# Performance work log

Hardware: AMD Instinct MI355X
Metric: run time of the kernel (lower is better)

Reference implementation:

```python
import jax, jax.numpy as jnp
import numpy as np

B, C, H, W = 16, 1024, 64, 64
NODE_H, NODE_W = 32, 32
N = NODE_H * NODE_W          # 1024 nodes
HID = 16                     # hidden_ch


def setup_inputs() -> dict:
    key = jax.random.key(0)
    k0, k1, k2 = jax.random.split(key, 3)
    feature = jax.random.normal(k0, (B, C, H, W), dtype=jnp.float32)
    mu_w = jax.random.normal(k1, (HID, C, 3, 3), dtype=jnp.float32) * 0.02
    mu_b = jnp.zeros((HID,), dtype=jnp.float32)
    lv_w = jax.random.normal(k2, (HID, C, 1, 1), dtype=jnp.float32) * 0.02
    lv_b = jnp.zeros((HID,), dtype=jnp.float32)
    return {"feature": feature, "mu_w": mu_w, "mu_b": mu_b, "lv_w": lv_w, "lv_b": lv_b}


def _conv(x, w, b, pad):
    y = jax.lax.conv_general_dilated(
        x, w, window_strides=(1, 1), padding=pad,
        dimension_numbers=("NCHW", "OIHW", "NCHW"))
    return y + b[None, :, None, None]


def reference(feature, mu_w, mu_b, lv_w, lv_b):
    # AdaptiveAvgPool2d((32,32)) with H,W multiples of 32 == mean over 2x2 blocks
    nodes = feature.reshape(B, C, NODE_H, H // NODE_H, NODE_W, W // NODE_W).mean(axis=(3, 5))
    mu = _conv(nodes, mu_w, mu_b, "SAME")      # (B, HID, 32, 32), Dropout is identity at eval
    log_var = _conv(nodes, lv_w, lv_b, "VALID")  # 1x1 conv, pad 0

    # eval-mode reparameterize: z = mu; torch raw reshape (B,HID,32,32)->(B,N,HID)
    z = mu.reshape(B, N, HID)

    kl_loss = -(0.5 * N * HID) * jnp.mean(
        jnp.sum(1.0 + 2.0 * log_var - mu ** 2 - jnp.exp(log_var) ** 2, axis=1))

    A = jnp.einsum("bnc,bmc->bnm", z, z)       # (B, N, N)
    A = jax.nn.relu(A)
    Ad = jnp.diagonal(A, axis1=1, axis2=2)      # (B, N)
    sigma = jnp.sum(Ad, axis=1)                 # (B,)
    gamma = jnp.sqrt(1.0 + N / (sigma + 1e-7))[:, None, None]  # (B,1,1)
    dl_loss = -gamma * jnp.log(Ad + 1e-7).sum() / (B * N * N)  # (B,1,1), faithful to torch

    eye = jnp.eye(N, dtype=A.dtype)
    A = A + gamma * (Ad[:, :, None] * eye)      # batched diagflat scatter

    # Laplacian normalize with self loop
    A = A + eye[None]
    deg_inv_sqrt = (jnp.sum(A, axis=1) + 1e-5) ** -0.5          # (B, N)
    LA = deg_inv_sqrt[:, :, None] * A * deg_inv_sqrt[:, None, :]

    z_hat = mu.reshape(B, N, HID) * (1.0 - log_var.reshape(B, N, HID))
    z_hat = gamma * z_hat
    return (LA, z, z_hat, kl_loss, dl_loss)
```

## Files before the change

kernel.cpp:

```cpp
#include <hip/hip_runtime.h>

typedef short short8 __attribute__((ext_vector_type(8)));
typedef float f32x4 __attribute__((ext_vector_type(4)));
typedef unsigned short ushort4v __attribute__((ext_vector_type(4)));

#define ZOFF   16777216
#define ZHOFF  17039360
#define KLOFF  17301504
#define DLOFF  17301505
#define APK_U  16777216
#define LVPK_U 16924672
#define AD_W   0
#define DIS_W  16384
#define PART_W 32768
#define GAM_W  34816
#define PMU_W  65536
#define PLV_W  2162688
#define Z16F   3211264

__device__ __forceinline__ unsigned short f2bf(float f) {
    unsigned int u = __float_as_uint(f);
    unsigned int r = (u + 0x7fffu + ((u >> 16) & 1u)) >> 16;
    return (unsigned short)r;
}
__device__ __forceinline__ float bf2f(unsigned short u) {
    return __uint_as_float(((unsigned int)u) << 16);
}

__global__ __launch_bounds__(256) void pool_tr_kernel(const float* __restrict__ f,
        unsigned short* __restrict__ nT, const float* __restrict__ mu_w,
        const float* __restrict__ lv_w, unsigned short* __restrict__ apk,
        unsigned short* __restrict__ lvpk)
{
    __shared__ float pls[64 * 35];
    int blk = blockIdx.x;
    int b  = blk >> 9;
    int y  = (blk >> 4) & 31;
    int cb = blk & 15;
    int t  = threadIdx.x;
    int rr  = (t >> 4) & 1;
    int c16 = t & 15;
    int cho = t >> 5;
    #pragma unroll
    for (int k = 0; k < 8; ++k) {
        int ch = (k << 3) + cho;
        float4 v = ((const float4*)f)[
            ((((b << 10) + (cb << 6) + ch) << 6) + (y << 1) + rr) * 16 + c16];
        float h0 = v.x + v.y, h1 = v.z + v.w;
        float g0 = h0 + __shfl_xor(h0, 16);
        float g1 = h1 + __shfl_xor(h1, 16);
        if (rr == 0) {
            pls[ch * 35 + (c16 << 1)]     = 0.25f * g0;
            pls[ch * 35 + (c16 << 1) + 1] = 0.25f * g1;
        }
    }
    __syncthreads();
    int px = t >> 3, cg2 = t & 7;
    unsigned short o8[8];
    #pragma unroll
    for (int i = 0; i < 8; ++i) o8[i] = f2bf(pls[((cg2 << 3) + i) * 35 + px]);
    int ofs = ((((b << 10) + (y << 5) + px)) << 10) + (cb << 6) + (cg2 << 3);
    *(short8*)&nT[ofs] = *(short8*)o8;

    if (blk < 640) {
        int idx = blk * 256 + t;
        if (idx < 147456) {
            int tap = idx >> 14;
            int rem = idx & 16383;
            int ks = rem >> 9;
            int lane = (rem >> 3) & 63;
            int j = idx & 7;
            int o = lane & 15;
            int cc = (ks << 5) + ((lane >> 4) << 3) + j;
            apk[idx] = f2bf(mu_w[((o << 10) + cc) * 9 + tap]);
        } else {
            int i2 = idx - 147456;
            int ks = i2 >> 9;
            int lane = (i2 >> 3) & 63;
            int j = i2 & 7;
            int o = lane & 15;
            int cc = (ks << 5) + ((lane >> 4) << 3) + j;
            lvpk[i2] = f2bf(lv_w[(o << 10) + cc]);
        }
    }
}

__global__ __launch_bounds__(256) void conv_mfma(const unsigned short* __restrict__ nT,
        const unsigned short* __restrict__ apk, const unsigned short* __restrict__ lvpk,
        unsigned short* __restrict__ pmu, unsigned short* __restrict__ plv)
{
    __shared__ unsigned short st[6 * 34 * 40];
    int blk = blockIdx.x;
    int b  = blk >> 6;
    int yt = (blk >> 3) & 7;
    int kc = blk & 7;
    int y0 = yt << 2;
    int t  = threadIdx.x;
    int w  = t >> 6, l = t & 63;
    int px = l & 15, chg = l >> 4;
    f32x4 accm[2] = {{0,0,0,0},{0,0,0,0}};
    f32x4 accv[2] = {{0,0,0,0},{0,0,0,0}};

    if (t < 48) {
        int row = t >> 3, side = (t >> 2) & 1, quarter = t & 3;
        short8 z8 = {0,0,0,0,0,0,0,0};
        *(short8*)&st[(row * 34 + side * 33) * 40 + quarter * 8] = z8;
    }

    for (int s = 0; s < 4; ++s) {
        int ksg = (kc << 2) + s;
        int cs  = ksg << 5;
        __syncthreads();
        #pragma unroll
        for (int k2 = 0; k2 < 3; ++k2) {
            int q = t + (k2 << 8);
            int quarter = q & 3, x = (q >> 2) & 31, row = q >> 7;
            int yin = y0 - 1 + row;
            short8 v = {0,0,0,0,0,0,0,0};
            if (yin >= 0 && yin < 32)
                v = *(const short8*)&nT[(((b << 10) + (yin << 5) + x) << 10) + cs + quarter * 8];
            *(short8*)&st[(row * 34 + x + 1) * 40 + quarter * 8] = v;
        }
        __syncthreads();
        short8 bw[9], bvw;
        #pragma unroll
        for (int tap = 0; tap < 9; ++tap)
            bw[tap] = *(const short8*)&apk[((tap << 5) + ksg) * 512 + l * 8];
        bvw = *(const short8*)&lvpk[(ksg << 9) + l * 8];
        #pragma unroll
        for (int h = 0; h < 2; ++h) {
            short8 actr;
            #pragma unroll
            for (int ky = 0; ky < 3; ++ky) {
                int row = w + ky;
                #pragma unroll
                for (int kx = 0; kx < 3; ++kx) {
                    int xx = (h << 4) + px + kx;
                    short8 a = *(const short8*)&st[(row * 34 + xx) * 40 + chg * 8];
                    if (ky == 1 && kx == 1) actr = a;
                    accm[h] = __builtin_amdgcn_mfma_f32_16x16x32_bf16(a, bw[ky*3+kx], accm[h], 0, 0, 0);
                }
            }
            accv[h] = __builtin_amdgcn_mfma_f32_16x16x32_bf16(actr, bvw, accv[h], 0, 0, 0);
        }
    }
    int o = px;
    #pragma unroll
    for (int h = 0; h < 2; ++h) {
        int x = (h << 4) + (chg << 2);
        int idx = (((kc << 4) + b) << 14) + (o << 10) + ((y0 + w) << 5) + x;
        ushort4v m16, v16;
        #pragma unroll
        for (int j = 0; j < 4; ++j) { m16[j] = f2bf(accm[h][j]); v16[j] = f2bf(accv[h][j]); }
        *(ushort4v*)&pmu[idx] = m16;
        *(ushort4v*)&plv[idx] = v16;
    }
}

__global__ __launch_bounds__(256) void stats_kernel(const unsigned short* __restrict__ pmu,
        const unsigned short* __restrict__ plv, const float* __restrict__ mu_b,
        const float* __restrict__ lv_b, float* __restrict__ z,
        float* __restrict__ lvout, float* __restrict__ ws)
{
    __shared__ float smu[16 * 68], slv[16 * 68];
    __shared__ float red[3][4];
    unsigned short* z16 = (unsigned short*)(ws + Z16F);
    int blk = blockIdx.x;
    int b = blk >> 4, ng = blk & 15;
    int t = threadIdx.x;
    {
        int o = t >> 4, f4c = t & 15;
        int base = (b << 14) + (o << 10) + (ng << 6) + (f4c << 2);
        f32x4 m = {0,0,0,0}, lv = {0,0,0,0};
        #pragma unroll
        for (int kc = 0; kc < 8; ++kc) {
            ushort4v mu16 = *(const ushort4v*)(pmu + (kc << 18) + base);
            ushort4v lv16 = *(const ushort4v*)(plv + (kc << 18) + base);
            #pragma unroll
            for (int c = 0; c < 4; ++c) {
                m[c]  += bf2f(mu16[c]);
                lv[c] += bf2f(lv16[c]);
            }
        }
        float mb = mu_b[o], lb = lv_b[o];
        #pragma unroll
        for (int c = 0; c < 4; ++c) {
            smu[o * 68 + (f4c << 2) + c] = m[c] + mb;
            slv[o * 68 + (f4c << 2) + c] = lv[c] + lb;
        }
    }
    __syncthreads();
    int node2 = t >> 2, og = t & 3;
    f32x4 zm, zl;
    float ad = 0.f, klp = 0.f;
    #pragma unroll
    for (int c = 0; c < 4; ++c) {
        float mm = smu[((og << 2) + c) * 68 + node2];
        float ll = slv[((og << 2) + c) * 68 + node2];
        zm[c] = mm; zl[c] = ll;
        ad  += mm * mm;
        klp += 1.0f + 2.0f * ll - mm * mm - expf(2.0f * ll);
    }
    int zofs = (b << 14) + (((ng << 6) + node2) << 4) + (og << 2);
    *(f32x4*)(z + zofs)     = zm;
    *(f32x4*)(lvout + zofs) = zl;
    ushort4v z16v;
    #pragma unroll
    for (int c = 0; c < 4; ++c) z16v[c] = f2bf(zm[c]);
    *(ushort4v*)&z16[zofs] = z16v;
    ad  += __shfl_xor(ad, 1);  ad  += __shfl_xor(ad, 2);
    klp += __shfl_xor(klp, 1); klp += __shfl_xor(klp, 2);
    float lg = logf(ad + 1e-7f);
    if (og == 0) ws[AD_W + (b << 10) + (ng << 6) + node2] = ad;
    float sgc = (og == 0) ? ad  : 0.f;
    float klc = (og == 0) ? klp : 0.f;
    float lgc = (og == 0) ? lg  : 0.f;
    #pragma unroll
    for (int off = 32; off > 0; off >>= 1) {
        sgc += __shfl_down(sgc, off);
        klc += __shfl_down(klc, off);
        lgc += __shfl_down(lgc, off);
    }
    int wv = t >> 6;
    if ((t & 63) == 0) { red[0][wv] = sgc; red[1][wv] = klc; red[2][wv] = lgc; }
    __syncthreads();
    if (t == 0) {
        ws[PART_W + (blk << 2) + 0] = red[0][0] + red[0][1] + red[0][2] + red[0][3];
        ws[PART_W + (blk << 2) + 1] = red[1][0] + red[1][1] + red[1][2] + red[1][3];
        ws[PART_W + (blk << 2) + 2] = red[2][0] + red[2][1] + red[2][2] + red[2][3];
    }
}

__global__ __launch_bounds__(256) void deg_kernel(const float* __restrict__ z,
        float* __restrict__ lvzh, float* __restrict__ ws, float* __restrict__ out)
{
    __shared__ float redk[4], redl[4], fin[2];
    const unsigned short* z16 = (const unsigned short*)(ws + Z16F);
    int blk = blockIdx.x;
    int b  = blk >> 4;
    int n0 = (blk & 15) << 6;
    int t  = threadIdx.x;
    int w  = t >> 6, l = t & 63;
    int lo = l & 15, hi = l >> 4;
    float sg16 = 0.f;
    #pragma unroll
    for (int g = 0; g < 16; ++g) sg16 += ws[PART_W + (((b << 4) + g) << 2)];
    float gam = sqrtf(1.0f + 1024.0f / (sg16 + 1e-7f));
    #pragma unroll
    for (int e = 0; e < 4; ++e) {
        int zi = (b << 14) + (n0 << 4) + (e << 8) + t;
        lvzh[zi] = gam * z[zi] * (1.0f - lvzh[zi]);
    }
    const unsigned short* zb = z16 + (b << 14);
    int rn = n0 + (w << 4);
    short8 afrag = {0,0,0,0,0,0,0,0};
    if (l < 32) afrag = *(const short8*)&zb[((rn + lo) << 4) + (hi << 3)];
    f32x4 rs = {0.f, 0.f, 0.f, 0.f};
    #pragma unroll 4
    for (int mt = 0; mt < 64; ++mt) {
        short8 bfrag = {0,0,0,0,0,0,0,0};
        if (l < 32) bfrag = *(const short8*)&zb[(((mt << 4) + lo) << 4) + (hi << 3)];
        f32x4 d = {0.f, 0.f, 0.f, 0.f};
        d = __builtin_amdgcn_mfma_f32_16x16x32_bf16(afrag, bfrag, d, 0, 0, 0);
        #pragma unroll
        for (int jj = 0; jj < 4; ++jj) rs[jj] += fmaxf(d[jj], 0.f);
    }
    #pragma unroll
    for (int m = 1; m < 16; m <<= 1) {
        #pragma unroll
        for (int jj = 0; jj < 4; ++jj) rs[jj] += __shfl_xor(rs[jj], m);
    }
    if (lo == 0) {
        #pragma unroll
        for (int jj = 0; jj < 4; ++jj) {
            int n = rn + (hi << 2) + jj;
            float deg = rs[jj] + gam * ws[AD_W + (b << 10) + n] + 1.0f;
            ws[DIS_W + (b << 10) + n] = rsqrtf(deg + 1e-5f);
        }
    }
    if (blk == 0) {
        float kl = ws[PART_W + (t << 2) + 1];
        float lg = ws[PART_W + (t << 2) + 2];
        #pragma unroll
        for (int off = 32; off > 0; off >>= 1) {
            kl += __shfl_down(kl, off);
            lg += __shfl_down(lg, off);
        }
        if ((t & 63) == 0) { redk[t >> 6] = kl; redl[t >> 6] = lg; }
        __syncthreads();
        if (t == 0) {
            fin[0] = redk[0] + redk[1] + redk[2] + redk[3];
            fin[1] = redl[0] + redl[1] + redl[2] + redl[3];
            out[KLOFF] = -0.5f * fin[0];
        }
        __syncthreads();
        if (t < 16) {
            float s = 0.f;
            #pragma unroll
            for (int g = 0; g < 16; ++g) s += ws[PART_W + (((t << 4) + g) << 2)];
            float gm = sqrtf(1.0f + 1024.0f / (s + 1e-7f));
            ws[GAM_W + t] = gm;
            out[DLOFF + t] = -gm * fin[1] / 16777216.0f;
        }
    }
}

__global__ __launch_bounds__(256) void la_kernel(const float* __restrict__ ws,
        float* __restrict__ LA)
{
    __shared__ float dan[64], dbm[64], sAd[64];
    const unsigned short* z16 = (const unsigned short*)(ws + Z16F);
    int b    = blockIdx.x >> 8;
    int tile = blockIdx.x & 255;
    int n0 = (tile >> 4) * 64;
    int m0 = (tile & 15) * 64;
    int t  = threadIdx.x;
    int w  = t >> 6, l = t & 63;
    const float* dis = ws + DIS_W + (b << 10);
    if (t < 64)       dan[t]      = dis[n0 + t];
    else if (t < 128) dbm[t - 64] = dis[m0 + (t - 64)];
    else if (t < 192) sAd[t - 128] = (n0 == m0) ? ws[AD_W + (b << 10) + n0 + (t - 128)] : 0.0f;
    __syncthreads();
    float g = ws[GAM_W + b];
    const unsigned short* zb = z16 + (b << 14);
    int rn = n0 + (w << 4);
    int lo = l & 15, hi = l >> 4;
    short8 afrag = {0,0,0,0,0,0,0,0};
    if (l < 32) afrag = *(const short8*)&zb[((rn + lo) << 4) + (hi << 3)];
    #pragma unroll
    for (int j = 0; j < 4; ++j) {
        int rm = m0 + (j << 4);
        short8 bfrag = {0,0,0,0,0,0,0,0};
        if (l < 32) bfrag = *(const short8*)&zb[((rm + lo) << 4) + (hi << 3)];
        f32x4 d = {0.f, 0.f, 0.f, 0.f};
        d = __builtin_amdgcn_mfma_f32_16x16x32_bf16(afrag, bfrag, d, 0, 0, 0);
        int c = rm + lo;
        float dm = dbm[(j << 4) + lo];
        #pragma unroll
        for (int jj = 0; jj < 4; ++jj) {
            int r = rn + (hi << 2) + jj;
            float v = fmaxf(d[jj], 0.f);
            if (r == c) v += g * sAd[r - n0] + 1.0f;
            float dn = dan[(w << 4) + (hi << 2) + jj];
            LA[((size_t)b << 20) + ((size_t)r << 10) + c] = dn * dm * v;
        }
    }
}

extern "C" void kernel_launch(void* const* d_in, const int* in_sizes, int n_in,
                              void* d_out, int out_size, void* d_ws, size_t ws_size,
                              hipStream_t stream) {
    const float* feature = (const float*)d_in[0];
    const float* mu_w    = (const float*)d_in[1];
    const float* mu_b    = (const float*)d_in[2];
    const float* lv_w    = (const float*)d_in[3];
    const float* lv_b    = (const float*)d_in[4];
    float* out = (float*)d_out;
    float* ws  = (float*)d_ws;
    unsigned short* nT   = (unsigned short*)d_out;
    unsigned short* apk  = nT + APK_U;
    unsigned short* lvpk = nT + LVPK_U;
    unsigned short* pmu16 = (unsigned short*)(ws + PMU_W);
    unsigned short* plv16 = (unsigned short*)(ws + PLV_W);

    pool_tr_kernel<<<8192, 256, 0, stream>>>(feature, nT, mu_w, lv_w, apk, lvpk);
    conv_mfma<<<1024, 256, 0, stream>>>(nT, apk, lvpk, pmu16, plv16);
    stats_kernel<<<256, 256, 0, stream>>>(pmu16, plv16, mu_b, lv_b,
                                          out + ZOFF, out + ZHOFF, ws);
    deg_kernel<<<256, 256, 0, stream>>>(out + ZOFF, out + ZHOFF, ws, out);
    la_kernel<<<4096, 256, 0, stream>>>(ws, out);
}
```

Before: 111.7 us.

## Double-buffer conv input tiles in LDS and halve the channel split

```diff
diff --git a/kernel.cpp b/kernel.cpp
--- a/kernel.cpp
+++ b/kernel.cpp
@@ -89,11 +89,11 @@
         const unsigned short* __restrict__ apk, const unsigned short* __restrict__ lvpk,
         unsigned short* __restrict__ pmu, unsigned short* __restrict__ plv)
 {
-    __shared__ unsigned short st[6 * 34 * 40];
+    __shared__ unsigned short st[2][6 * 34 * 40];
     int blk = blockIdx.x;
-    int b  = blk >> 6;
-    int yt = (blk >> 3) & 7;
-    int kc = blk & 7;
+    int b  = blk >> 5;
+    int yt = (blk >> 2) & 7;
+    int kc = blk & 3;
     int y0 = yt << 2;
     int t  = threadIdx.x;
     int w  = t >> 6, l = t & 63;
@@ -104,24 +104,44 @@
     if (t < 48) {
         int row = t >> 3, side = (t >> 2) & 1, quarter = t & 3;
         short8 z8 = {0,0,0,0,0,0,0,0};
-        *(short8*)&st[(row * 34 + side * 33) * 40 + quarter * 8] = z8;
-    }
-
-    for (int s = 0; s < 4; ++s) {
-        int ksg = (kc << 2) + s;
-        int cs  = ksg << 5;
-        __syncthreads();
+        *(short8*)&st[0][(row * 34 + side * 33) * 40 + quarter * 8] = z8;
+        *(short8*)&st[1][(row * 34 + side * 33) * 40 + quarter * 8] = z8;
+    }
+
+    int qr[3], qx[3], qq[3];
+    bool ok[3];
+    #pragma unroll
+    for (int k2 = 0; k2 < 3; ++k2) {
+        int q = t + (k2 << 8);
+        qq[k2] = q & 3; qx[k2] = (q >> 2) & 31; qr[k2] = q >> 7;
+        int yin = y0 - 1 + qr[k2];
+        ok[k2] = (yin >= 0 && yin < 32);
+    }
+    const unsigned short* nb = nT + ((size_t)b << 20);
+    const short8 z8 = {0,0,0,0,0,0,0,0};
+    short8 r[3];
+    {
+        int cs = (kc << 8);
         #pragma unroll
         for (int k2 = 0; k2 < 3; ++k2) {
-            int q = t + (k2 << 8);
-            int quarter = q & 3, x = (q >> 2) & 31, row = q >> 7;
-            int yin = y0 - 1 + row;
-            short8 v = {0,0,0,0,0,0,0,0};
-            if (yin >= 0 && yin < 32)
-                v = *(const short8*)&nT[(((b << 10) + (yin << 5) + x) << 10) + cs + quarter * 8];
-            *(short8*)&st[(row * 34 + x + 1) * 40 + quarter * 8] = v;
-        }
-        __syncthreads();
+            r[k2] = z8;
+            if (ok[k2]) r[k2] = *(const short8*)&nb[((((y0 - 1 + qr[k2]) << 5) + qx[k2]) << 10) + cs + qq[k2] * 8];
+            *(short8*)&st[0][(qr[k2] * 34 + qx[k2] + 1) * 40 + qq[k2] * 8] = r[k2];
+        }
+    }
+    __syncthreads();
+
+    for (int s = 0; s < 8; ++s) {
+        int ksg = (kc << 3) + s;
+        int cur = s & 1;
+        if (s < 7) {
+            int cs = (ksg + 1) << 5;
+            #pragma unroll
+            for (int k2 = 0; k2 < 3; ++k2) {
+                r[k2] = z8;
+                if (ok[k2]) r[k2] = *(const short8*)&nb[((((y0 - 1 + qr[k2]) << 5) + qx[k2]) << 10) + cs + qq[k2] * 8];
+            }
+        }
         short8 bw[9], bvw;
         #pragma unroll
         for (int tap = 0; tap < 9; ++tap)
@@ -136,13 +156,19 @@
                 #pragma unroll
                 for (int kx = 0; kx < 3; ++kx) {
                     int xx = (h << 4) + px + kx;
-                    short8 a = *(const short8*)&st[(row * 34 + xx) * 40 + chg * 8];
+                    short8 a = *(const short8*)&st[cur][(row * 34 + xx) * 40 + chg * 8];
                     if (ky == 1 && kx == 1) actr = a;
                     accm[h] = __builtin_amdgcn_mfma_f32_16x16x32_bf16(a, bw[ky*3+kx], accm[h], 0, 0, 0);
                 }
             }
             accv[h] = __builtin_amdgcn_mfma_f32_16x16x32_bf16(actr, bvw, accv[h], 0, 0, 0);
         }
+        if (s < 7) {
+            #pragma unroll
+            for (int k2 = 0; k2 < 3; ++k2)
+                *(short8*)&st[cur ^ 1][(qr[k2] * 34 + qx[k2] + 1) * 40 + qq[k2] * 8] = r[k2];
+        }
+        __syncthreads();
     }
     int o = px;
     #pragma unroll
@@ -173,7 +199,7 @@
         int base = (b << 14) + (o << 10) + (ng << 6) + (f4c << 2);
         f32x4 m = {0,0,0,0}, lv = {0,0,0,0};
         #pragma unroll
-        for (int kc = 0; kc < 8; ++kc) {
+        for (int kc = 0; kc < 4; ++kc) {
             ushort4v mu16 = *(const ushort4v*)(pmu + (kc << 18) + base);
             ushort4v lv16 = *(const ushort4v*)(plv + (kc << 18) + base);
             #pragma unroll
@@ -364,7 +390,7 @@
     unsigned short* plv16 = (unsigned short*)(ws + PLV_W);
 
     pool_tr_kernel<<<8192, 256, 0, stream>>>(feature, nT, mu_w, lv_w, apk, lvpk);
-    conv_mfma<<<1024, 256, 0, stream>>>(nT, apk, lvpk, pmu16, plv16);
+    conv_mfma<<<512, 256, 0, stream>>>(nT, apk, lvpk, pmu16, plv16);
     stats_kernel<<<256, 256, 0, stream>>>(pmu16, plv16, mu_b, lv_b,
                                           out + ZOFF, out + ZHOFF, ws);
     deg_kernel<<<256, 256, 0, stream>>>(out + ZOFF, out + ZHOFF, ws, out);
```

Result: slower. 116.2 us (+4.0%).
